# Kernel optimization log

Hardware: AMD Instinct MI355X
Metric: run time of the kernel (lower is better)

Reference implementation:

```python
import jax, jax.numpy as jnp
import numpy as np

N_NODES = 50000
N_EDGES = 800000
IN_FEAT = 128
HID = 128
OUT = 10
N_GRAPHS = 128
BN_EPS = 1e-5


def setup_inputs() -> dict:
    key = jax.random.key(0)
    ks = jax.random.split(key, 16)
    inp = {
        "n_feat": jax.random.normal(ks[0], (N_NODES, IN_FEAT), dtype=jnp.float32),
        "src": jax.random.randint(ks[1], (N_EDGES,), 0, N_NODES),
        "dst": jax.random.randint(ks[2], (N_EDGES,), 0, N_NODES),
        "graph_ids": jnp.sort(jax.random.randint(ks[3], (N_NODES,), 0, N_GRAPHS)),
        # GraphConv weights (DGL layout: weight [in, out], bias [out])
        "W1": jax.random.normal(ks[4], (IN_FEAT, HID), dtype=jnp.float32) / np.sqrt(IN_FEAT),
        "b1": jnp.zeros((HID,), dtype=jnp.float32),
        "W2": jax.random.normal(ks[5], (HID, HID), dtype=jnp.float32) / np.sqrt(HID),
        "b2": jnp.zeros((HID,), dtype=jnp.float32),
        # BatchNorm1d affine params
        "gamma": jnp.ones((HID,), dtype=jnp.float32),
        "beta": jnp.zeros((HID,), dtype=jnp.float32),
        # MLP head
        "fc1_w": jax.random.normal(ks[6], (HID, HID), dtype=jnp.float32) / np.sqrt(HID),
        "fc1_b": jnp.zeros((HID,), dtype=jnp.float32),
        "fc2_w": jax.random.normal(ks[7], (HID, OUT), dtype=jnp.float32) / np.sqrt(HID),
        "fc2_b": jnp.zeros((OUT,), dtype=jnp.float32),
    }
    return inp


def _graph_conv(x, W, b, src, dst, inv_sqrt_out, inv_sqrt_in):
    # DGL GraphConv, norm='both': h = D_in^{-1/2} A D_out^{-1/2} x W + b
    h = x * inv_sqrt_out[:, None]          # [N, d_in]
    h = h @ W                              # [N, d_out] (project before gather: fewer bytes moved)
    agg = jax.ops.segment_sum(h[src], dst, num_segments=N_NODES)  # gather + scatter-add
    return agg * inv_sqrt_in[:, None] + b


def reference(n_feat, src, dst, graph_ids, W1, b1, W2, b2, gamma, beta,
              fc1_w, fc1_b, fc2_w, fc2_b):
    ones_e = jnp.ones((N_EDGES,), dtype=jnp.float32)
    deg_out = jnp.clip(jax.ops.segment_sum(ones_e, src, num_segments=N_NODES), 1.0)
    deg_in = jnp.clip(jax.ops.segment_sum(ones_e, dst, num_segments=N_NODES), 1.0)
    inv_sqrt_out = jax.lax.rsqrt(deg_out)
    inv_sqrt_in = jax.lax.rsqrt(deg_in)

    x = jax.nn.relu(_graph_conv(n_feat, W1, b1, src, dst, inv_sqrt_out, inv_sqrt_in))
    # dropout is identity in eval mode
    x = jax.nn.relu(_graph_conv(x, W2, b2, src, dst, inv_sqrt_out, inv_sqrt_in))

    # SumPooling over graphs
    embedding = jax.ops.segment_sum(x, graph_ids, num_segments=N_GRAPHS)  # [B, HID]

    # BatchNorm1d (training-mode batch stats, biased variance like torch)
    mu = jnp.mean(embedding, axis=0)
    var = jnp.mean(jnp.square(embedding - mu), axis=0)
    h = gamma * (embedding - mu) * jax.lax.rsqrt(var + BN_EPS) + beta

    h = jax.nn.relu(h @ fc1_w + fc1_b)
    logits = h @ fc2_w + fc2_b
    return embedding, jax.nn.log_softmax(logits, axis=-1)
```

## Files before the change

### kernel.cpp

```cpp
#include <hip/hip_runtime.h>
#include <hip/hip_bf16.h>
#include <math.h>

#define N_NODES 50000
#define N_EDGES 800000
#define HID 128
#define N_GRAPHS 128
#define OUTC 10
#define BN_EPS 1e-5f

#define SCAN_B 256
#define N_SCAN_BLOCKS ((N_NODES + SCAN_B - 1) / SCAN_B)

#define POOL_CHUNK 32
#define N_POOL_BLOCKS ((N_NODES + POOL_CHUNK - 1) / POOL_CHUNK)

#define HB 80
#define HWORDS (N_NODES / 2)
#define HR_B 128
#define HR_BLOCKS ((HWORDS + HR_B - 1) / HR_B)

#define EPAD 8
#define E_SRC_CAP (N_EDGES + N_NODES * EPAD)

#define LDA 136

typedef short short8 __attribute__((ext_vector_type(8)));
typedef float floatx4 __attribute__((ext_vector_type(4)));

template <typename T, typename F>
__device__ inline T bitcast(F f) {
    union { F a; T b; } u;
    u.a = f;
    return u.b;
}

__global__ __launch_bounds__(1024) void hist_part_kernel(const int* __restrict__ src,
                                                         const int* __restrict__ dst,
                                                         unsigned int* __restrict__ part,
                                                         const float* __restrict__ W1,
                                                         const float* __restrict__ W2,
                                                         unsigned short* __restrict__ Wp) {
    if (blockIdx.x == 2 * HB) {
        for (int q = threadIdx.x; q < 4096; q += 1024) {
            int wi = q >> 11;
            const float* __restrict__ W = wi ? W2 : W1;
            int t2 = q & 2047;
            int tile = t2 >> 6, lane = t2 & 63;
            int kc = tile >> 3, nt = tile & 7;
            int n = lane & 15, quad = lane >> 4;
            unsigned short v[8];
#pragma unroll
            for (int j = 0; j < 8; j++) {
                int k = kc * 32 + quad * 8 + j;
                v[j] = __hip_bfloat16_raw(__float2bfloat16(W[k * HID + nt * 16 + n])).x;
            }
            *(uint4*)&Wp[(size_t)q * 8] = *(uint4*)v;
        }
        return;
    }
    __shared__ unsigned int h[HWORDS];
    for (int i = threadIdx.x; i < HWORDS; i += 1024) h[i] = 0;
    __syncthreads();
    int half = (blockIdx.x >= HB) ? 1 : 0;
    const int* __restrict__ idx = half ? dst : src;
    int b = blockIdx.x - half * HB;
    for (int e = b * 1024 + threadIdx.x; e < N_EDGES; e += HB * 1024) {
        int v = idx[e];
        atomicAdd(&h[v >> 1], 1u << ((v & 1) << 4));
    }
    __syncthreads();
    unsigned int* __restrict__ out = part + (size_t)blockIdx.x * HWORDS;
    for (int i = threadIdx.x; i < HWORDS; i += 1024) out[i] = h[i];
}

__global__ __launch_bounds__(HR_B) void hist_reduce_kernel(unsigned int* __restrict__ part,
                                                           int* __restrict__ cnt_in,
                                                           float* __restrict__ inv_out,
                                                           float* __restrict__ inv_in,
                                                           int* __restrict__ bsum) {
    int w = blockIdx.x * HR_B + threadIdx.x;
    int padsum = 0;
    if (w < HWORDS) {
        unsigned int s = 0, d = 0;
        for (int b = 0; b < HB; b++) {
            s += part[(size_t)b * HWORDS + w];
            unsigned int c = part[(size_t)(b + HB) * HWORDS + w];
            part[(size_t)(b + HB) * HWORDS + w] = d;
            d += c;
        }
        int i0 = w * 2, i1 = i0 + 1;
        int so0 = (int)(s & 0xFFFFu), so1 = (int)(s >> 16);
        int di0 = (int)(d & 0xFFFFu), di1 = (int)(d >> 16);
        cnt_in[i0] = di0;
        cnt_in[i1] = di1;
        inv_out[i0] = rsqrtf(fmaxf((float)so0, 1.0f));
        inv_out[i1] = rsqrtf(fmaxf((float)so1, 1.0f));
        inv_in[i0] = rsqrtf(fmaxf((float)di0, 1.0f));
        inv_in[i1] = rsqrtf(fmaxf((float)di1, 1.0f));
        padsum = ((di0 + EPAD - 1) & ~(EPAD - 1)) + ((di1 + EPAD - 1) & ~(EPAD - 1));
    }
    __shared__ int red[HR_B];
    red[threadIdx.x] = padsum;
    __syncthreads();
    for (int o = HR_B / 2; o > 0; o >>= 1) {
        if (threadIdx.x < o) red[threadIdx.x] += red[threadIdx.x + o];
        __syncthreads();
    }
    if (threadIdx.x == 0) bsum[blockIdx.x] = red[0];
}

__global__ void scan_bsum_kernel(const int* __restrict__ bsum, int* __restrict__ boff) {
    __shared__ int part[SCAN_B];
    int t = threadIdx.x;
    int v = (t < N_SCAN_BLOCKS) ? bsum[t] : 0;
    part[t] = v;
    __syncthreads();
    for (int off = 1; off < SCAN_B; off <<= 1) {
        int u = (t >= off) ? part[t - off] : 0;
        __syncthreads();
        part[t] += u;
        __syncthreads();
    }
    boff[t] = part[t] - v;
}

__global__ void scan_write_kernel(const int* __restrict__ cnt, const int* __restrict__ boff,
                                  int* __restrict__ row_ptr, int* __restrict__ edge_src) {
    __shared__ int part[SCAN_B];
    int t = threadIdx.x;
    int i = blockIdx.x * SCAN_B + t;
    int raw = (i < N_NODES) ? cnt[i] : 0;
    int v = (raw + EPAD - 1) & ~(EPAD - 1);
    part[t] = v;
    __syncthreads();
    for (int off = 1; off < SCAN_B; off <<= 1) {
        int u = (t >= off) ? part[t - off] : 0;
        __syncthreads();
        part[t] += u;
        __syncthreads();
    }
    if (i < N_NODES) {
        int ex = part[t] - v + boff[blockIdx.x];
        row_ptr[i] = ex;
        for (int p = ex + raw; p < ex + v; p++) edge_src[p] = N_NODES;
        if (i == N_NODES - 1) row_ptr[N_NODES] = ex + v;
    }
}

__global__ __launch_bounds__(1024) void csr_fill_kernel(const int* __restrict__ src,
                                                        const int* __restrict__ dst,
                                                        const unsigned int* __restrict__ part,
                                                        const int* __restrict__ row_ptr,
                                                        int* __restrict__ edge_src) {
    __shared__ unsigned int loc[HWORDS];
    int b = blockIdx.x;
    const unsigned int* __restrict__ off = part + (size_t)(b + HB) * HWORDS;
    for (int i = threadIdx.x; i < HWORDS; i += 1024) loc[i] = off[i];
    __syncthreads();
    for (int e = b * 1024 + threadIdx.x; e < N_EDGES; e += HB * 1024) {
        int d = dst[e];
        unsigned int old = atomicAdd(&loc[d >> 1], 1u << ((d & 1) << 4));
        int local = (d & 1) ? (int)(old >> 16) : (int)(old & 0xFFFFu);
        edge_src[row_ptr[d] + local] = src[e];
    }
}

__global__ __launch_bounds__(256) void matmul_kernel(const float* __restrict__ X,
                                                     const float* __restrict__ scale,
                                                     const unsigned short* __restrict__ Wp,
                                                     __hip_bfloat16* __restrict__ Y) {
    __shared__ unsigned short xs[64 * LDA];
    int tid = threadIdx.x;
    int row0 = blockIdx.x * 64;

    for (int j = 0; j < 8; j++) {
        int idx4 = j * 256 + tid;
        int r = idx4 >> 5;
        int col = (idx4 & 31) * 4;
        int rg = row0 + r;
        float4 v = make_float4(0.f, 0.f, 0.f, 0.f);
        if (rg < N_NODES) {
            v = *(const float4*)&X[(size_t)rg * HID + col];
            float sc = scale[rg];
            v.x *= sc; v.y *= sc; v.z *= sc; v.w *= sc;
        }
        unsigned short o[4];
        o[0] = __hip_bfloat16_raw(__float2bfloat16(v.x)).x;
        o[1] = __hip_bfloat16_raw(__float2bfloat16(v.y)).x;
        o[2] = __hip_bfloat16_raw(__float2bfloat16(v.z)).x;
        o[3] = __hip_bfloat16_raw(__float2bfloat16(v.w)).x;
        *(ushort4*)&xs[r * LDA + col] = *(ushort4*)o;
    }
    __syncthreads();

    int wave = tid >> 6, lane = tid & 63;
    int m = lane & 15, quad = lane >> 4;
    int rowl = wave * 16;

    short8 a[4];
#pragma unroll
    for (int kc = 0; kc < 4; kc++)
        a[kc] = bitcast<short8>(*(const uint4*)&xs[(rowl + m) * LDA + kc * 32 + quad * 8]);

    floatx4 acc[8];
#pragma unroll
    for (int nt = 0; nt < 8; nt++) acc[nt] = (floatx4){0.f, 0.f, 0.f, 0.f};

#pragma unroll
    for (int nt = 0; nt < 8; nt++) {
#pragma unroll
        for (int kc = 0; kc < 4; kc++) {
            short8 bfr = bitcast<short8>(
                *(const uint4*)&Wp[((size_t)(kc * 8 + nt) * 64 + lane) * 8]);
            acc[nt] = __builtin_amdgcn_mfma_f32_16x16x32_bf16(a[kc], bfr, acc[nt], 0, 0, 0);
        }
    }

#pragma unroll
    for (int nt = 0; nt < 8; nt++) {
#pragma unroll
        for (int i = 0; i < 4; i++) {
            int rg = row0 + rowl + quad * 4 + i;
            if (rg < N_NODES + 1) {
                Y[(size_t)rg * HID + nt * 16 + m] = __float2bfloat16(acc[nt][i]);
            }
        }
    }
}

__global__ __launch_bounds__(256) void agg_kernel(const __hip_bfloat16* __restrict__ Y,
                                                  const int* __restrict__ edge_src,
                                                  const int* __restrict__ row_ptr,
                                                  const float* __restrict__ inv_in,
                                                  const float* __restrict__ bias,
                                                  float* __restrict__ Xout) {
    const uint4* __restrict__ Yq = (const uint4*)Y;
    int wave = threadIdx.x >> 6;
    int lane = threadIdx.x & 63;
    int n = blockIdx.x * 4 + wave;
    if (n >= N_NODES) return;
    int beg = row_ptr[n], end = row_ptr[n + 1];
    int esub = lane >> 4;
    int f16  = lane & 15;
    float acc[8] = {};
    for (int base = beg; base < end; base += 64) {
        int mm = min(64, end - base);
        int idx = (lane < mm) ? edge_src[base + lane] : N_NODES;
        for (int j = 0; j < mm; j += 8) {
            int s0 = __shfl(idx, j + esub);
            int s1 = __shfl(idx, j + 4 + esub);
            uint4 u0 = Yq[s0 * (HID / 8) + f16];
            uint4 u1 = Yq[s1 * (HID / 8) + f16];
            acc[0] += __uint_as_float(u0.x << 16); acc[1] += __uint_as_float(u0.x & 0xFFFF0000u);
            acc[2] += __uint_as_float(u0.y << 16); acc[3] += __uint_as_float(u0.y & 0xFFFF0000u);
            acc[4] += __uint_as_float(u0.z << 16); acc[5] += __uint_as_float(u0.z & 0xFFFF0000u);
            acc[6] += __uint_as_float(u0.w << 16); acc[7] += __uint_as_float(u0.w & 0xFFFF0000u);
            acc[0] += __uint_as_float(u1.x << 16); acc[1] += __uint_as_float(u1.x & 0xFFFF0000u);
            acc[2] += __uint_as_float(u1.y << 16); acc[3] += __uint_as_float(u1.y & 0xFFFF0000u);
            acc[4] += __uint_as_float(u1.z << 16); acc[5] += __uint_as_float(u1.z & 0xFFFF0000u);
            acc[6] += __uint_as_float(u1.w << 16); acc[7] += __uint_as_float(u1.w & 0xFFFF0000u);
        }
    }
#pragma unroll
    for (int i = 0; i < 8; i++) {
        acc[i] += __shfl_xor(acc[i], 16);
        acc[i] += __shfl_xor(acc[i], 32);
    }
    if (lane < 16) {
        float si = inv_in[n];
        int f0 = f16 * 8;
        float4 b0 = *(const float4*)&bias[f0];
        float4 b1 = *(const float4*)&bias[f0 + 4];
        float4 o0, o1;
        o0.x = fmaxf(acc[0] * si + b0.x, 0.f);
        o0.y = fmaxf(acc[1] * si + b0.y, 0.f);
        o0.z = fmaxf(acc[2] * si + b0.z, 0.f);
        o0.w = fmaxf(acc[3] * si + b0.w, 0.f);
        o1.x = fmaxf(acc[4] * si + b1.x, 0.f);
        o1.y = fmaxf(acc[5] * si + b1.y, 0.f);
        o1.z = fmaxf(acc[6] * si + b1.z, 0.f);
        o1.w = fmaxf(acc[7] * si + b1.w, 0.f);
        *(float4*)&Xout[(size_t)n * HID + f0] = o0;
        *(float4*)&Xout[(size_t)n * HID + f0 + 4] = o1;
    }
}

__global__ __launch_bounds__(64) void pool_kernel(const float* __restrict__ X,
                                                  const int* __restrict__ gid,
                                                  float* __restrict__ emb) {
    int lane = threadIdx.x;
    int n0 = blockIdx.x * POOL_CHUNK;
    int n1 = min(n0 + POOL_CHUNK, N_NODES);
    if (n0 >= N_NODES) return;
    int g_cur = gid[n0];
    float ax = 0.f, ay = 0.f;
    for (int n = n0; n < n1; n++) {
        int g = gid[n];
        if (g != g_cur) {
            atomicAdd(&emb[g_cur * HID + lane * 2], ax);
            atomicAdd(&emb[g_cur * HID + lane * 2 + 1], ay);
            ax = 0.f; ay = 0.f;
            g_cur = g;
        }
        float2 v = *(const float2*)&X[(size_t)n * HID + lane * 2];
        ax += v.x;
        ay += v.y;
    }
    atomicAdd(&emb[g_cur * HID + lane * 2], ax);
    atomicAdd(&emb[g_cur * HID + lane * 2 + 1], ay);
}

__global__ __launch_bounds__(128) void head_fused_kernel(const float* __restrict__ emb,
                                                         const float* __restrict__ gamma,
                                                         const float* __restrict__ beta,
                                                         const float* __restrict__ fc1_w,
                                                         const float* __restrict__ fc1_b,
                                                         const float* __restrict__ fc2_w,
                                                         const float* __restrict__ fc2_b,
                                                         float* __restrict__ out) {
    int r = blockIdx.x, f = threadIdx.x;
    float s = 0.f;
    for (int row = 0; row < N_GRAPHS; row++) s += emb[row * HID + f];
    float mu = s * (1.f / N_GRAPHS);
    float v = 0.f;
    for (int row = 0; row < N_GRAPHS; row++) {
        float d = emb[row * HID + f] - mu;
        v += d * d;
    }
    v *= (1.f / N_GRAPHS);
    float sc = gamma[f] * rsqrtf(v + BN_EPS);
    float sh = beta[f] - mu * sc;

    __shared__ float xr[HID];
    xr[f] = emb[r * HID + f] * sc + sh;
    __syncthreads();
    float acc = fc1_b[f];
    for (int k = 0; k < HID; k++) acc += xr[k] * fc1_w[k * HID + f];
    __shared__ float hr[HID];
    hr[f] = fmaxf(acc, 0.f);
    __syncthreads();

    __shared__ float logits[OUTC];
    __shared__ float mstat[2];
    if (f < OUTC) {
        float a = fc2_b[f];
        for (int k = 0; k < HID; k++) a += hr[k] * fc2_w[k * OUTC + f];
        logits[f] = a;
    }
    __syncthreads();
    if (f == 0) {
        float m = logits[0];
        for (int o = 1; o < OUTC; o++) m = fmaxf(m, logits[o]);
        float sum = 0.f;
        for (int o = 0; o < OUTC; o++) sum += expf(logits[o] - m);
        mstat[0] = m;
        mstat[1] = logf(sum);
    }
    __syncthreads();
    if (f < OUTC) out[r * OUTC + f] = logits[f] - mstat[0] - mstat[1];
}

extern "C" void kernel_launch(void* const* d_in, const int* in_sizes, int n_in,
                              void* d_out, int out_size, void* d_ws, size_t ws_size,
                              hipStream_t stream) {
    const float* n_feat = (const float*)d_in[0];
    const int*   src    = (const int*)d_in[1];
    const int*   dst    = (const int*)d_in[2];
    const int*   gid    = (const int*)d_in[3];
    const float* W1     = (const float*)d_in[4];
    const float* b1     = (const float*)d_in[5];
    const float* W2     = (const float*)d_in[6];
    const float* b2     = (const float*)d_in[7];
    const float* gamma  = (const float*)d_in[8];
    const float* beta   = (const float*)d_in[9];
    const float* fc1_w  = (const float*)d_in[10];
    const float* fc1_b  = (const float*)d_in[11];
    const float* fc2_w  = (const float*)d_in[12];
    const float* fc2_b  = (const float*)d_in[13];

    char* wsb = (char*)d_ws;
    size_t off = 0;
    auto alloc = [&](size_t bytes) -> void* {
        void* p = wsb + off;
        off += (bytes + 255) & ~(size_t)255;
        return p;
    };
    int*   cnt_in  = (int*)alloc((size_t)N_NODES * 4);
    int*   row_ptr = (int*)alloc((size_t)(N_NODES + 1) * 4);
    int*   e_src   = (int*)alloc((size_t)E_SRC_CAP * 4);
    float* inv_out = (float*)alloc((size_t)N_NODES * 4);
    float* inv_in  = (float*)alloc((size_t)N_NODES * 4);
    void*  ybuf    = alloc((size_t)2 * HB * HWORDS * 4);
    float* X       = (float*)alloc((size_t)N_NODES * HID * 4);
    unsigned short* Wp = (unsigned short*)alloc((size_t)2 * 32 * 64 * 8 * 2);
    int*   bsum    = (int*)alloc((size_t)SCAN_B * 4);
    int*   boff    = (int*)alloc((size_t)SCAN_B * 4);

    unsigned int*   part = (unsigned int*)ybuf;
    __hip_bfloat16* Y    = (__hip_bfloat16*)ybuf;

    float* emb_out = (float*)d_out;
    float* lsm_out = emb_out + N_GRAPHS * HID;

    hipMemsetAsync(emb_out, 0, (size_t)N_GRAPHS * HID * 4, stream);

    hist_part_kernel<<<2 * HB + 1, 1024, 0, stream>>>(src, dst, part, W1, W2, Wp);
    hist_reduce_kernel<<<HR_BLOCKS, HR_B, 0, stream>>>(part, cnt_in, inv_out, inv_in, bsum);
    scan_bsum_kernel<<<1, SCAN_B, 0, stream>>>(bsum, boff);
    scan_write_kernel<<<N_SCAN_BLOCKS, SCAN_B, 0, stream>>>(cnt_in, boff, row_ptr, e_src);
    csr_fill_kernel<<<HB, 1024, 0, stream>>>(src, dst, part, row_ptr, e_src);

    matmul_kernel<<<(N_NODES + 64) / 64, 256, 0, stream>>>(n_feat, inv_out, Wp, Y);
    agg_kernel<<<(N_NODES + 3) / 4, 256, 0, stream>>>(Y, e_src, row_ptr, inv_in, b1, X);
    matmul_kernel<<<(N_NODES + 64) / 64, 256, 0, stream>>>(X, inv_out, Wp + (size_t)32 * 64 * 8, Y);
    agg_kernel<<<(N_NODES + 3) / 4, 256, 0, stream>>>(Y, e_src, row_ptr, inv_in, b2, X);

    pool_kernel<<<N_POOL_BLOCKS, 64, 0, stream>>>(X, gid, emb_out);
    head_fused_kernel<<<N_GRAPHS, HID, 0, stream>>>(emb_out, gamma, beta, fc1_w, fc1_b,
                                                    fc2_w, fc2_b, lsm_out);
}
```

Before: 255.4 us.

## Fuse degree reduce with atomic-offset scan and store layer-1 output in bf16

The histogram reduce, block-sum scan and scan-write kernels become one kernel. It does a block-local scan and takes its global base from an atomic counter, so rows are placed in arbitrary block order and each node gets explicit row_ptr/row_end arrays. The first aggregation layer now writes its activations as bf16, and the second matmul reads bf16 directly, halving that intermediate traffic. This drops two launches and extra passes over the count array, at the cost of one added memset, a non-monotone CSR layout and one more bf16 rounding step (the matmul already rounded its input to bf16).

```diff
diff --git a/kernel.cpp b/kernel.cpp
--- a/kernel.cpp
+++ b/kernel.cpp
@@ -8,9 +8,6 @@
 #define N_GRAPHS 128
 #define OUTC 10
 #define BN_EPS 1e-5f
-
-#define SCAN_B 256
-#define N_SCAN_BLOCKS ((N_NODES + SCAN_B - 1) / SCAN_B)
 
 #define POOL_CHUNK 32
 #define N_POOL_BLOCKS ((N_NODES + POOL_CHUNK - 1) / POOL_CHUNK)
@@ -74,13 +71,16 @@
     for (int i = threadIdx.x; i < HWORDS; i += 1024) out[i] = h[i];
 }
 
-__global__ __launch_bounds__(HR_B) void hist_reduce_kernel(unsigned int* __restrict__ part,
-                                                           int* __restrict__ cnt_in,
-                                                           float* __restrict__ inv_out,
-                                                           float* __restrict__ inv_in,
-                                                           int* __restrict__ bsum) {
-    int w = blockIdx.x * HR_B + threadIdx.x;
-    int padsum = 0;
+__global__ __launch_bounds__(HR_B) void hist_reduce_scan_kernel(unsigned int* __restrict__ part,
+                                                                float* __restrict__ inv_out,
+                                                                float* __restrict__ inv_in,
+                                                                int* __restrict__ row_ptr,
+                                                                int* __restrict__ row_end,
+                                                                int* __restrict__ edge_src,
+                                                                int* __restrict__ counter) {
+    int t = threadIdx.x;
+    int w = blockIdx.x * HR_B + t;
+    int raw0 = 0, raw1 = 0, p0 = 0, p1 = 0;
     if (w < HWORDS) {
         unsigned int s = 0, d = 0;
         for (int b = 0; b < HB; b++) {
@@ -91,60 +91,38 @@
         }
         int i0 = w * 2, i1 = i0 + 1;
         int so0 = (int)(s & 0xFFFFu), so1 = (int)(s >> 16);
-        int di0 = (int)(d & 0xFFFFu), di1 = (int)(d >> 16);
-        cnt_in[i0] = di0;
-        cnt_in[i1] = di1;
+        raw0 = (int)(d & 0xFFFFu);
+        raw1 = (int)(d >> 16);
         inv_out[i0] = rsqrtf(fmaxf((float)so0, 1.0f));
         inv_out[i1] = rsqrtf(fmaxf((float)so1, 1.0f));
-        inv_in[i0] = rsqrtf(fmaxf((float)di0, 1.0f));
-        inv_in[i1] = rsqrtf(fmaxf((float)di1, 1.0f));
-        padsum = ((di0 + EPAD - 1) & ~(EPAD - 1)) + ((di1 + EPAD - 1) & ~(EPAD - 1));
-    }
-    __shared__ int red[HR_B];
-    red[threadIdx.x] = padsum;
-    __syncthreads();
-    for (int o = HR_B / 2; o > 0; o >>= 1) {
-        if (threadIdx.x < o) red[threadIdx.x] += red[threadIdx.x + o];
+        inv_in[i0] = rsqrtf(fmaxf((float)raw0, 1.0f));
+        inv_in[i1] = rsqrtf(fmaxf((float)raw1, 1.0f));
+        p0 = (raw0 + EPAD - 1) & ~(EPAD - 1);
+        p1 = (raw1 + EPAD - 1) & ~(EPAD - 1);
+    }
+    __shared__ int sc[HR_B];
+    __shared__ int base_sh;
+    int tsum = p0 + p1;
+    sc[t] = tsum;
+    __syncthreads();
+    for (int o = 1; o < HR_B; o <<= 1) {
+        int u = (t >= o) ? sc[t - o] : 0;
         __syncthreads();
-    }
-    if (threadIdx.x == 0) bsum[blockIdx.x] = red[0];
-}
-
-__global__ void scan_bsum_kernel(const int* __restrict__ bsum, int* __restrict__ boff) {
-    __shared__ int part[SCAN_B];
-    int t = threadIdx.x;
-    int v = (t < N_SCAN_BLOCKS) ? bsum[t] : 0;
-    part[t] = v;
-    __syncthreads();
-    for (int off = 1; off < SCAN_B; off <<= 1) {
-        int u = (t >= off) ? part[t - off] : 0;
+        sc[t] += u;
         __syncthreads();
-        part[t] += u;
-        __syncthreads();
-    }
-    boff[t] = part[t] - v;
-}
-
-__global__ void scan_write_kernel(const int* __restrict__ cnt, const int* __restrict__ boff,
-                                  int* __restrict__ row_ptr, int* __restrict__ edge_src) {
-    __shared__ int part[SCAN_B];
-    int t = threadIdx.x;
-    int i = blockIdx.x * SCAN_B + t;
-    int raw = (i < N_NODES) ? cnt[i] : 0;
-    int v = (raw + EPAD - 1) & ~(EPAD - 1);
-    part[t] = v;
-    __syncthreads();
-    for (int off = 1; off < SCAN_B; off <<= 1) {
-        int u = (t >= off) ? part[t - off] : 0;
-        __syncthreads();
-        part[t] += u;
-        __syncthreads();
-    }
-    if (i < N_NODES) {
-        int ex = part[t] - v + boff[blockIdx.x];
-        row_ptr[i] = ex;
-        for (int p = ex + raw; p < ex + v; p++) edge_src[p] = N_NODES;
-        if (i == N_NODES - 1) row_ptr[N_NODES] = ex + v;
+    }
+    if (t == HR_B - 1) base_sh = atomicAdd(counter, sc[t]);
+    __syncthreads();
+    int ex = base_sh + sc[t] - tsum;
+    if (w < HWORDS) {
+        int i0 = w * 2, i1 = i0 + 1;
+        int st0 = ex, st1 = ex + p0;
+        row_ptr[i0] = st0;
+        row_end[i0] = st0 + p0;
+        row_ptr[i1] = st1;
+        row_end[i1] = st1 + p1;
+        for (int p = st0 + raw0; p < st0 + p0; p++) edge_src[p] = N_NODES;
+        for (int p = st1 + raw1; p < st1 + p1; p++) edge_src[p] = N_NODES;
     }
 }
 
@@ -166,7 +144,8 @@
     }
 }
 
-__global__ __launch_bounds__(256) void matmul_kernel(const float* __restrict__ X,
+template <int IN_BF16>
+__global__ __launch_bounds__(256) void matmul_kernel(const void* __restrict__ Xin,
                                                      const float* __restrict__ scale,
                                                      const unsigned short* __restrict__ Wp,
                                                      __hip_bfloat16* __restrict__ Y) {
@@ -174,23 +153,48 @@
     int tid = threadIdx.x;
     int row0 = blockIdx.x * 64;
 
-    for (int j = 0; j < 8; j++) {
-        int idx4 = j * 256 + tid;
-        int r = idx4 >> 5;
-        int col = (idx4 & 31) * 4;
-        int rg = row0 + r;
-        float4 v = make_float4(0.f, 0.f, 0.f, 0.f);
-        if (rg < N_NODES) {
-            v = *(const float4*)&X[(size_t)rg * HID + col];
-            float sc = scale[rg];
-            v.x *= sc; v.y *= sc; v.z *= sc; v.w *= sc;
-        }
-        unsigned short o[4];
-        o[0] = __hip_bfloat16_raw(__float2bfloat16(v.x)).x;
-        o[1] = __hip_bfloat16_raw(__float2bfloat16(v.y)).x;
-        o[2] = __hip_bfloat16_raw(__float2bfloat16(v.z)).x;
-        o[3] = __hip_bfloat16_raw(__float2bfloat16(v.w)).x;
-        *(ushort4*)&xs[r * LDA + col] = *(ushort4*)o;
+    if (IN_BF16) {
+        const unsigned int* __restrict__ X = (const unsigned int*)Xin;
+        for (int j = 0; j < 4; j++) {
+            int idx8 = j * 256 + tid;
+            int r = idx8 >> 4;
+            int col = (idx8 & 15) * 8;
+            int rg = row0 + r;
+            unsigned short o[8] = {};
+            if (rg < N_NODES) {
+                uint4 u = *(const uint4*)&X[(size_t)rg * (HID / 2) + col / 2];
+                float sc = scale[rg];
+                unsigned int uw[4] = {u.x, u.y, u.z, u.w};
+#pragma unroll
+                for (int q = 0; q < 4; q++) {
+                    float lo = __uint_as_float(uw[q] << 16) * sc;
+                    float hi = __uint_as_float(uw[q] & 0xFFFF0000u) * sc;
+                    o[q * 2]     = __hip_bfloat16_raw(__float2bfloat16(lo)).x;
+                    o[q * 2 + 1] = __hip_bfloat16_raw(__float2bfloat16(hi)).x;
+                }
+            }
+            *(uint4*)&xs[r * LDA + col] = *(uint4*)o;
+        }
+    } else {
+        const float* __restrict__ X = (const float*)Xin;
+        for (int j = 0; j < 8; j++) {
+            int idx4 = j * 256 + tid;
+            int r = idx4 >> 5;
+            int col = (idx4 & 31) * 4;
+            int rg = row0 + r;
+            float4 v = make_float4(0.f, 0.f, 0.f, 0.f);
+            if (rg < N_NODES) {
+                v = *(const float4*)&X[(size_t)rg * HID + col];
+                float sc = scale[rg];
+                v.x *= sc; v.y *= sc; v.z *= sc; v.w *= sc;
+            }
+            unsigned short o[4];
+            o[0] = __hip_bfloat16_raw(__float2bfloat16(v.x)).x;
+            o[1] = __hip_bfloat16_raw(__float2bfloat16(v.y)).x;
+            o[2] = __hip_bfloat16_raw(__float2bfloat16(v.z)).x;
+            o[3] = __hip_bfloat16_raw(__float2bfloat16(v.w)).x;
+            *(ushort4*)&xs[r * LDA + col] = *(ushort4*)o;
+        }
     }
     __syncthreads();
 
@@ -229,18 +233,20 @@
     }
 }
 
+template <int OUT_BF16>
 __global__ __launch_bounds__(256) void agg_kernel(const __hip_bfloat16* __restrict__ Y,
                                                   const int* __restrict__ edge_src,
                                                   const int* __restrict__ row_ptr,
+                                                  const int* __restrict__ row_end,
                                                   const float* __restrict__ inv_in,
                                                   const float* __restrict__ bias,
-                                                  float* __restrict__ Xout) {
+                                                  void* __restrict__ Xout) {
     const uint4* __restrict__ Yq = (const uint4*)Y;
     int wave = threadIdx.x >> 6;
     int lane = threadIdx.x & 63;
     int n = blockIdx.x * 4 + wave;
     if (n >= N_NODES) return;
-    int beg = row_ptr[n], end = row_ptr[n + 1];
+    int beg = row_ptr[n], end = row_end[n];
     int esub = lane >> 4;
     int f16  = lane & 15;
     float acc[8] = {};
@@ -272,17 +278,26 @@
         int f0 = f16 * 8;
         float4 b0 = *(const float4*)&bias[f0];
         float4 b1 = *(const float4*)&bias[f0 + 4];
-        float4 o0, o1;
-        o0.x = fmaxf(acc[0] * si + b0.x, 0.f);
-        o0.y = fmaxf(acc[1] * si + b0.y, 0.f);
-        o0.z = fmaxf(acc[2] * si + b0.z, 0.f);
-        o0.w = fmaxf(acc[3] * si + b0.w, 0.f);
-        o1.x = fmaxf(acc[4] * si + b1.x, 0.f);
-        o1.y = fmaxf(acc[5] * si + b1.y, 0.f);
-        o1.z = fmaxf(acc[6] * si + b1.z, 0.f);
-        o1.w = fmaxf(acc[7] * si + b1.w, 0.f);
-        *(float4*)&Xout[(size_t)n * HID + f0] = o0;
-        *(float4*)&Xout[(size_t)n * HID + f0 + 4] = o1;
+        float o[8];
+        o[0] = fmaxf(acc[0] * si + b0.x, 0.f);
+        o[1] = fmaxf(acc[1] * si + b0.y, 0.f);
+        o[2] = fmaxf(acc[2] * si + b0.z, 0.f);
+        o[3] = fmaxf(acc[3] * si + b0.w, 0.f);
+        o[4] = fmaxf(acc[4] * si + b1.x, 0.f);
+        o[5] = fmaxf(acc[5] * si + b1.y, 0.f);
+        o[6] = fmaxf(acc[6] * si + b1.z, 0.f);
+        o[7] = fmaxf(acc[7] * si + b1.w, 0.f);
+        if (OUT_BF16) {
+            unsigned short ob[8];
+#pragma unroll
+            for (int i = 0; i < 8; i++)
+                ob[i] = __hip_bfloat16_raw(__float2bfloat16(o[i])).x;
+            *(uint4*)&((unsigned short*)Xout)[(size_t)n * HID + f0] = *(uint4*)ob;
+        } else {
+            float* Xf = (float*)Xout;
+            *(float4*)&Xf[(size_t)n * HID + f0] = make_float4(o[0], o[1], o[2], o[3]);
+            *(float4*)&Xf[(size_t)n * HID + f0 + 4] = make_float4(o[4], o[5], o[6], o[7]);
+        }
     }
 }
 
@@ -386,16 +401,16 @@
         off += (bytes + 255) & ~(size_t)255;
         return p;
     };
-    int*   cnt_in  = (int*)alloc((size_t)N_NODES * 4);
-    int*   row_ptr = (int*)alloc((size_t)(N_NODES + 1) * 4);
+    int*   row_ptr = (int*)alloc((size_t)N_NODES * 4);
+    int*   row_end = (int*)alloc((size_t)N_NODES * 4);
     int*   e_src   = (int*)alloc((size_t)E_SRC_CAP * 4);
     float* inv_out = (float*)alloc((size_t)N_NODES * 4);
     float* inv_in  = (float*)alloc((size_t)N_NODES * 4);
     void*  ybuf    = alloc((size_t)2 * HB * HWORDS * 4);
     float* X       = (float*)alloc((size_t)N_NODES * HID * 4);
+    unsigned short* Xb = (unsigned short*)alloc((size_t)N_NODES * HID * 2);
     unsigned short* Wp = (unsigned short*)alloc((size_t)2 * 32 * 64 * 8 * 2);
-    int*   bsum    = (int*)alloc((size_t)SCAN_B * 4);
-    int*   boff    = (int*)alloc((size_t)SCAN_B * 4);
+    int*   counter = (int*)alloc(256);
 
     unsigned int*   part = (unsigned int*)ybuf;
     __hip_bfloat16* Y    = (__hip_bfloat16*)ybuf;
@@ -404,17 +419,20 @@
     float* lsm_out = emb_out + N_GRAPHS * HID;
 
     hipMemsetAsync(emb_out, 0, (size_t)N_GRAPHS * HID * 4, stream);
+    hipMemsetAsync(counter, 0, 4, stream);
 
     hist_part_kernel<<<2 * HB + 1, 1024, 0, stream>>>(src, dst, part, W1, W2, Wp);
-    hist_reduce_kernel<<<HR_BLOCKS, HR_B, 0, stream>>>(part, cnt_in, inv_out, inv_in, bsum);
-    scan_bsum_kernel<<<1, SCAN_B, 0, stream>>>(bsum, boff);
-    scan_write_kernel<<<N_SCAN_BLOCKS, SCAN_B, 0, stream>>>(cnt_in, boff, row_ptr, e_src);
+    hist_reduce_scan_kernel<<<HR_BLOCKS, HR_B, 0, stream>>>(part, inv_out, inv_in, row_ptr,
+                                                            row_end, e_src, counter);
     csr_fill_kernel<<<HB, 1024, 0, stream>>>(src, dst, part, row_ptr, e_src);
 
-    matmul_kernel<<<(N_NODES + 64) / 64, 256, 0, stream>>>(n_feat, inv_out, Wp, Y);
-    agg_kernel<<<(N_NODES + 3) / 4, 256, 0, stream>>>(Y, e_src, row_ptr, inv_in, b1, X);
-    matmul_kernel<<<(N_NODES + 64) / 64, 256, 0, stream>>>(X, inv_out, Wp + (size_t)32 * 64 * 8, Y);
-    agg_kernel<<<(N_NODES + 3) / 4, 256, 0, stream>>>(Y, e_src, row_ptr, inv_in, b2, X);
+    matmul_kernel<0><<<(N_NODES + 64) / 64, 256, 0, stream>>>(n_feat, inv_out, Wp, Y);
+    agg_kernel<1><<<(N_NODES + 3) / 4, 256, 0, stream>>>(Y, e_src, row_ptr, row_end,
+                                                         inv_in, b1, Xb);
+    matmul_kernel<1><<<(N_NODES + 64) / 64, 256, 0, stream>>>(Xb, inv_out,
+                                                              Wp + (size_t)32 * 64 * 8, Y);
+    agg_kernel<0><<<(N_NODES + 3) / 4, 256, 0, stream>>>(Y, e_src, row_ptr, row_end,
+                                                         inv_in, b2, X);
 
     pool_kernel<<<N_POOL_BLOCKS, 64, 0, stream>>>(X, gid, emb_out);
     head_fused_kernel<<<N_GRAPHS, HID, 0, stream>>>(emb_out, gamma, beta, fc1_w, fc1_b,
```

Result: no change. 256.4 us (+0.4%).
